# Performance work log

Hardware: AMD Instinct MI355X
Metric: run time of the kernel (lower is better)

## Reference

```python
import jax, jax.numpy as jnp
import numpy as np

N_NODES = 100000
N_EDGES = 3200000
DROP_P = 0.5


def gcn_conv(x, W, b, src, dst, deg_inv_sqrt, n):
    # PyG GCNConv with self-loops already folded into (src, dst):
    # out[j] = sum_{(i->j)} dinv[i]*dinv[j] * (x W)[i] + b
    h = x @ W
    norm = deg_inv_sqrt[src] * deg_inv_sqrt[dst]          # [E+N]
    msg = h[src] * norm[:, None]                          # [E+N, d_out]
    out = jax.ops.segment_sum(msg, dst, num_segments=n)
    return out + b


def dropout(x, key, p=DROP_P):
    keep = jax.random.bernoulli(key, 1.0 - p, x.shape)
    return jnp.where(keep, x / (1.0 - p), 0.0)


def setup_inputs() -> dict:
    key = jax.random.key(0)
    ks = jax.random.split(key, 8)
    x = jax.random.normal(ks[0], (N_NODES, 64), dtype=jnp.float32)
    edge_index = jax.random.randint(ks[1], (2, N_EDGES), 0, N_NODES, dtype=jnp.int64)
    def glorot(k, fin, fout):
        lim = float(np.sqrt(6.0 / (fin + fout)))
        return jax.random.uniform(k, (fin, fout), jnp.float32, -lim, lim)
    return {
        "x": x,
        "edge_index": edge_index,
        "W1": glorot(ks[2], 64, 32), "b1": jnp.zeros((32,), jnp.float32),
        "W2": glorot(ks[3], 32, 64), "b2": jnp.zeros((64,), jnp.float32),
        "W3": glorot(ks[4], 64, 32), "b3": jnp.zeros((32,), jnp.float32),
    }


def reference(x, edge_index, W1, b1, W2, b2, W3, b3):
    n = x.shape[0]
    loops = jnp.arange(n, dtype=edge_index.dtype)
    src = jnp.concatenate([edge_index[0], loops])          # [E+N]
    dst = jnp.concatenate([edge_index[1], loops])
    deg = jax.ops.segment_sum(jnp.ones_like(dst, dtype=x.dtype), dst, num_segments=n)
    deg_inv_sqrt = jnp.where(deg > 0, jax.lax.rsqrt(deg), 0.0)

    dkey = jax.random.key(42)
    k1, k2 = jax.random.split(dkey)

    h = gcn_conv(x, W1, b1, src, dst, deg_inv_sqrt, n)
    h = jax.nn.celu(h)
    h = dropout(h, k1)
    h = gcn_conv(h, W2, b2, src, dst, deg_inv_sqrt, n)
    h = jax.nn.celu(h)
    h = dropout(h, k2)
    h = gcn_conv(h, W3, b3, src, dst, deg_inv_sqrt, n)
    return jax.nn.celu(h)
```

## Files before the change

kernel.cpp:

```cpp
#include <hip/hip_runtime.h>
#include <stdint.h>
#include <stddef.h>

typedef _Float16 half_t;
typedef _Float16 half4 __attribute__((ext_vector_type(4)));
typedef _Float16 half8 __attribute__((ext_vector_type(8)));

__host__ __device__ __forceinline__ uint32_t rotl32(uint32_t v, uint32_t r) {
  return (v << r) | (v >> (32u - r));
}

__host__ __device__ __forceinline__ void tf2x32(uint32_t k0, uint32_t k1,
                                                uint32_t x0, uint32_t x1,
                                                uint32_t& o0, uint32_t& o1) {
  uint32_t ks2 = k0 ^ k1 ^ 0x1BD11BDAu;
  x0 += k0; x1 += k1;
  x0 += x1; x1 = rotl32(x1, 13); x1 ^= x0;
  x0 += x1; x1 = rotl32(x1, 15); x1 ^= x0;
  x0 += x1; x1 = rotl32(x1, 26); x1 ^= x0;
  x0 += x1; x1 = rotl32(x1, 6);  x1 ^= x0;
  x0 += k1; x1 += ks2 + 1u;
  x0 += x1; x1 = rotl32(x1, 17); x1 ^= x0;
  x0 += x1; x1 = rotl32(x1, 29); x1 ^= x0;
  x0 += x1; x1 = rotl32(x1, 16); x1 ^= x0;
  x0 += x1; x1 = rotl32(x1, 24); x1 ^= x0;
  x0 += ks2; x1 += k0 + 2u;
  x0 += x1; x1 = rotl32(x1, 13); x1 ^= x0;
  x0 += x1; x1 = rotl32(x1, 15); x1 ^= x0;
  x0 += x1; x1 = rotl32(x1, 26); x1 ^= x0;
  x0 += x1; x1 = rotl32(x1, 6);  x1 ^= x0;
  x0 += k0; x1 += k1 + 3u;
  x0 += x1; x1 = rotl32(x1, 17); x1 ^= x0;
  x0 += x1; x1 = rotl32(x1, 29); x1 ^= x0;
  x0 += x1; x1 = rotl32(x1, 16); x1 ^= x0;
  x0 += x1; x1 = rotl32(x1, 24); x1 ^= x0;
  x0 += k1; x1 += ks2 + 4u;
  x0 += x1; x1 = rotl32(x1, 13); x1 ^= x0;
  x0 += x1; x1 = rotl32(x1, 15); x1 ^= x0;
  x0 += x1; x1 = rotl32(x1, 26); x1 ^= x0;
  x0 += x1; x1 = rotl32(x1, 6);  x1 ^= x0;
  x0 += ks2; x1 += k0 + 5u;
  o0 = x0; o1 = x1;
}

__device__ __forceinline__ bool tf_keep(uint32_t k0, uint32_t k1, uint32_t idx) {
  uint32_t o0, o1;
  tf2x32(k0, k1, 0u, idx, o0, o1);
  return ((o0 ^ o1) >> 31) == 0u;
}

#define CHUNK 4096
#define STASH 5120

__global__ __launch_bounds__(1024) void zero1024(uint32_t* __restrict__ p) {
  p[threadIdx.x] = 0u;
}

__global__ __launch_bounds__(1024) void k4_binhist(const int* __restrict__ src,
                                                   const int* __restrict__ dst,
                                                   uint32_t* __restrict__ tbl,
                                                   uint32_t* __restrict__ gbcnt,
                                                   uint32_t* __restrict__ staging,
                                                   int E, int NB) {
  __shared__ uint32_t lcur[1024];
  __shared__ uint32_t ls[1024];
  __shared__ uint32_t stage[CHUNK];
  int tid = threadIdx.x;
  lcur[tid] = 0u;
  __syncthreads();
  int base = blockIdx.x * CHUNK;
  int end = min(base + CHUNK, E);
  uint32_t dv[4], sv[4];
  int m = 0;
  for (int i = base + tid; i < end; i += 1024) {
    dv[m] = (uint32_t)dst[i];
    sv[m] = (uint32_t)src[i];
    ++m;
  }
  for (int q = 0; q < m; ++q) atomicAdd(&lcur[dv[q] >> 7], 1u);
  __syncthreads();
  uint32_t v = lcur[tid];
  ls[tid] = v;
  __syncthreads();
  for (int off = 1; off < 1024; off <<= 1) {
    uint32_t t = (tid >= off) ? ls[tid - off] : 0u;
    __syncthreads();
    if (tid >= off) ls[tid] += t;
    __syncthreads();
  }
  uint32_t excl = ls[tid] - v;
  if (tid < NB) {
    tbl[(size_t)blockIdx.x * NB + tid] = (excl << 16) | v;
    if (v) atomicAdd(&gbcnt[tid], v);
  }
  lcur[tid] = excl;
  __syncthreads();
  for (int q = 0; q < m; ++q) {
    uint32_t d = dv[q];
    uint32_t p = atomicAdd(&lcur[d >> 7], 1u);
    stage[p] = ((d & 127u) << 17) | sv[q];
  }
  __syncthreads();
  int cnt_total = end - base;
  uint32_t* outp = staging + (size_t)blockIdx.x * CHUNK;
  for (int i = tid; i < cnt_total; i += 1024) outp[i] = stage[i];
}

__global__ __launch_bounds__(1024) void k3_bscan(const uint32_t* __restrict__ gbcnt,
                                                 uint32_t* __restrict__ bbase, int NB) {
  __shared__ uint32_t s[1024];
  int i = threadIdx.x;
  uint32_t v = (i < NB) ? gbcnt[i] : 0u;
  s[i] = v;
  __syncthreads();
  for (int off = 1; off < 1024; off <<= 1) {
    uint32_t t = (i >= off) ? s[i - off] : 0u;
    __syncthreads();
    if (i >= off) s[i] += t;
    __syncthreads();
  }
  if (i < NB) bbase[i] = s[i] - v;
}

__global__ __launch_bounds__(1024) void k5_fin(
    const uint32_t* __restrict__ staging, const uint32_t* __restrict__ tbl,
    const uint32_t* __restrict__ bbase, uint32_t* __restrict__ rowp,
    float* __restrict__ dinv, uint32_t* __restrict__ esrc,
    int n, int E, int NBLK, int NB) {
  __shared__ uint32_t loff[1024];
  __shared__ uint32_t P[1025];
  __shared__ uint32_t ls[1024];
  __shared__ uint32_t stash[STASH];
  __shared__ uint32_t lc[128];
  __shared__ uint32_t sc[128];
  __shared__ uint32_t lcur[128];
  int tid = threadIdx.x;
  int b = blockIdx.x;
  if (tid < 128) lc[tid] = 0u;
  uint32_t packed = (tid < NBLK) ? tbl[(size_t)tid * NB + b] : 0u;
  uint32_t v = packed & 0xFFFFu;
  loff[tid] = packed >> 16;
  ls[tid] = v;
  __syncthreads();
  for (int off = 1; off < 1024; off <<= 1) {
    uint32_t t = (tid >= off) ? ls[tid - off] : 0u;
    __syncthreads();
    if (tid >= off) ls[tid] += t;
    __syncthreads();
  }
  P[tid] = ls[tid] - v;
  if (tid == 1023) P[1024] = ls[1023];
  __syncthreads();
  uint32_t total = P[NBLK];
  for (uint32_t q = (uint32_t)tid; q < total; q += 1024u) {
    int lo = 0, hi = NBLK;
    while (hi - lo > 1) {
      int mid = (lo + hi) >> 1;
      if (P[mid] <= q) lo = mid; else hi = mid;
    }
    uint32_t e = staging[(size_t)lo * CHUNK + loff[lo] + (q - P[lo])];
    if (q < (uint32_t)STASH) stash[q] = e;
    atomicAdd(&lc[e >> 17], 1u);
  }
  __syncthreads();
  uint32_t myc = (tid < 128) ? lc[tid] : 0u;
  if (tid < 128) sc[tid] = myc;
  __syncthreads();
  for (int off = 1; off < 128; off <<= 1) {
    uint32_t t = (tid < 128 && tid >= off) ? sc[tid - off] : 0u;
    __syncthreads();
    if (tid < 128 && tid >= off) sc[tid] += t;
    __syncthreads();
  }
  uint32_t s = bbase[b];
  if (tid < 128) {
    uint32_t gstart = s + sc[tid] - myc;
    int node = (b << 7) + tid;
    if (node < n) {
      rowp[node] = gstart;
      dinv[node] = 1.0f / sqrtf((float)(myc + 1u));
    }
    lcur[tid] = gstart;
  }
  if (b == 0 && tid == 0) rowp[n] = (uint32_t)E;
  __syncthreads();
  uint32_t lim = total < (uint32_t)STASH ? total : (uint32_t)STASH;
  for (uint32_t q = (uint32_t)tid; q < lim; q += 1024u) {
    uint32_t e = stash[q];
    uint32_t pos = atomicAdd(&lcur[e >> 17], 1u);
    esrc[pos] = e & 0x1FFFFu;
  }
  if (total > (uint32_t)STASH) {
    for (uint32_t q = (uint32_t)STASH + (uint32_t)tid; q < total; q += 1024u) {
      int lo = 0, hi = NBLK;
      while (hi - lo > 1) {
        int mid = (lo + hi) >> 1;
        if (P[mid] <= q) lo = mid; else hi = mid;
      }
      uint32_t e = staging[(size_t)lo * CHUNK + loff[lo] + (q - P[lo])];
      uint32_t pos = atomicAdd(&lcur[e >> 17], 1u);
      esrc[pos] = e & 0x1FFFFu;
    }
  }
}

__global__ __launch_bounds__(256) void gemm_n64_k32(
    const float* __restrict__ X, const float* __restrict__ W,
    const float* __restrict__ dinv, half_t* __restrict__ out16, int n) {
  __shared__ float Ws[64 * 32];
  __shared__ float Xs[32 * 68];
  int tid = threadIdx.x;
  {
    const float4* Wv = (const float4*)W;
    float4* Wsv = (float4*)Ws;
    Wsv[tid] = Wv[tid];
    Wsv[tid + 256] = Wv[tid + 256];
  }
  int row0 = blockIdx.x * 32;
  {
    const float4* Xv = (const float4*)(X + (size_t)row0 * 64);
    int lim = (n - row0) * 16;
    float4 z = make_float4(0.f, 0.f, 0.f, 0.f);
    int i0 = tid, i1 = tid + 256;
    float4 v0 = (i0 < lim) ? Xv[i0] : z;
    float4 v1 = (i1 < lim) ? Xv[i1] : z;
    *(float4*)(Xs + (i0 >> 4) * 68 + ((i0 & 15) << 2)) = v0;
    *(float4*)(Xs + (i1 >> 4) * 68 + ((i1 & 15) << 2)) = v1;
  }
  __syncthreads();
  int r = tid >> 3;
  int c4 = (tid & 7) << 2;
  int row = row0 + r;
  if (row >= n) return;
  float4 acc = make_float4(0.f, 0.f, 0.f, 0.f);
#pragma unroll
  for (int k = 0; k < 64; k += 4) {
    float4 xv = *(const float4*)(Xs + r * 68 + k);
    float4 w0 = *(const float4*)(Ws + (k + 0) * 32 + c4);
    float4 w1 = *(const float4*)(Ws + (k + 1) * 32 + c4);
    float4 w2 = *(const float4*)(Ws + (k + 2) * 32 + c4);
    float4 w3 = *(const float4*)(Ws + (k + 3) * 32 + c4);
    acc.x = fmaf(xv.x, w0.x, acc.x); acc.y = fmaf(xv.x, w0.y, acc.y);
    acc.z = fmaf(xv.x, w0.z, acc.z); acc.w = fmaf(xv.x, w0.w, acc.w);
    acc.x = fmaf(xv.y, w1.x, acc.x); acc.y = fmaf(xv.y, w1.y, acc.y);
    acc.z = fmaf(xv.y, w1.z, acc.z); acc.w = fmaf(xv.y, w1.w, acc.w);
    acc.x = fmaf(xv.z, w2.x, acc.x); acc.y = fmaf(xv.z, w2.y, acc.y);
    acc.z = fmaf(xv.z, w2.z, acc.z); acc.w = fmaf(xv.z, w2.w, acc.w);
    acc.x = fmaf(xv.w, w3.x, acc.x); acc.y = fmaf(xv.w, w3.y, acc.y);
    acc.z = fmaf(xv.w, w3.z, acc.z); acc.w = fmaf(xv.w, w3.w, acc.w);
  }
  float dj = dinv[row];
  half4 h;
  h.x = (half_t)(acc.x * dj); h.y = (half_t)(acc.y * dj);
  h.z = (half_t)(acc.z * dj); h.w = (half_t)(acc.w * dj);
  *(half4*)(out16 + (size_t)row * 32 + c4) = h;
}

__global__ __launch_bounds__(256) void gemm_k32_n64_act(
    const float* __restrict__ X, const float* __restrict__ W,
    const float* __restrict__ bias, float* __restrict__ out,
    uint32_t k0, uint32_t k1, int n) {
  __shared__ float Ws[32 * 64];
  __shared__ float Xs[16 * 36];
  int tid = threadIdx.x;
  {
    const float4* Wv = (const float4*)W;
    float4* Wsv = (float4*)Ws;
    Wsv[tid] = Wv[tid];
    Wsv[tid + 256] = Wv[tid + 256];
  }
  int row0 = blockIdx.x * 16;
  if (tid < 128) {
    const float4* Xv = (const float4*)(X + (size_t)row0 * 32);
    int lim = (n - row0) * 8;
    float4 z = make_float4(0.f, 0.f, 0.f, 0.f);
    float4 v = (tid < lim) ? Xv[tid] : z;
    *(float4*)(Xs + (tid >> 3) * 36 + ((tid & 7) << 2)) = v;
  }
  __syncthreads();
  int r = tid >> 4;
  int c4 = (tid & 15) << 2;
  int row = row0 + r;
  if (row >= n) return;
  float4 acc = make_float4(0.f, 0.f, 0.f, 0.f);
#pragma unroll
  for (int k = 0; k < 32; k += 4) {
    float4 xv = *(const float4*)(Xs + r * 36 + k);
    float4 w0 = *(const float4*)(Ws + (k + 0) * 64 + c4);
    float4 w1 = *(const float4*)(Ws + (k + 1) * 64 + c4);
    float4 w2 = *(const float4*)(Ws + (k + 2) * 64 + c4);
    float4 w3 = *(const float4*)(Ws + (k + 3) * 64 + c4);
    acc.x = fmaf(xv.x, w0.x, acc.x); acc.y = fmaf(xv.x, w0.y, acc.y);
    acc.z = fmaf(xv.x, w0.z, acc.z); acc.w = fmaf(xv.x, w0.w, acc.w);
    acc.x = fmaf(xv.y, w1.x, acc.x); acc.y = fmaf(xv.y, w1.y, acc.y);
    acc.z = fmaf(xv.y, w1.z, acc.z); acc.w = fmaf(xv.y, w1.w, acc.w);
    acc.x = fmaf(xv.z, w2.x, acc.x); acc.y = fmaf(xv.z, w2.y, acc.y);
    acc.z = fmaf(xv.z, w2.z, acc.z); acc.w = fmaf(xv.z, w2.w, acc.w);
    acc.x = fmaf(xv.w, w3.x, acc.x); acc.y = fmaf(xv.w, w3.y, acc.y);
    acc.z = fmaf(xv.w, w3.z, acc.z); acc.w = fmaf(xv.w, w3.w, acc.w);
  }
  float4 bv = *(const float4*)(bias + c4);
  float vv[4] = {acc.x + bv.x, acc.y + bv.y, acc.z + bv.z, acc.w + bv.w};
  uint32_t base = (uint32_t)row * 64u + (uint32_t)c4;
#pragma unroll
  for (int q = 0; q < 4; ++q) {
    float v = vv[q];
    v = v > 0.f ? v : expm1f(v);
    vv[q] = tf_keep(k0, k1, base + q) ? v * 2.f : 0.f;
  }
  *(float4*)(out + (size_t)row * 64 + c4) = make_float4(vv[0], vv[1], vv[2], vv[3]);
}

__global__ __launch_bounds__(256) void gather_fin(
    const half_t* __restrict__ hs, const uint32_t* __restrict__ rowp,
    const uint32_t* __restrict__ esrc, const float* __restrict__ dinv,
    const float* __restrict__ bias, float* __restrict__ outf,
    half_t* __restrict__ outh, int n, int mode, uint32_t k0, uint32_t k1,
    float fone) {
  __shared__ __align__(16) float ldsred[256];
  (void)fone;
  int tid = threadIdx.x;
  int gt = blockIdx.x * 256 + tid;
  int j = gt >> 5;
  int g = tid >> 5;
  int l = tid & 31;
  int eslot = l >> 2;
  int chunk = l & 3;
  float acc[8] = {0.f, 0.f, 0.f, 0.f, 0.f, 0.f, 0.f, 0.f};
  uint32_t e0 = 0, deg = 0;
  float selfv = 0.f, dj = 0.f;
  if (j < n) {
    e0 = rowp[j];
    deg = rowp[j + 1] - e0;
    selfv = (float)hs[(size_t)j * 32 + l];
    dj = dinv[j];
  }
  const half_t* hp = hs + (size_t)(chunk << 3);
  const half8 hz = {(half_t)0, (half_t)0, (half_t)0, (half_t)0,
                    (half_t)0, (half_t)0, (half_t)0, (half_t)0};
  for (uint32_t base = 0; base < deg; base += 64u) {
    uint32_t rem = deg - base;
    if (rem > 64u) rem = 64u;
    uint32_t li0 = (uint32_t)l < rem ? (uint32_t)l : rem - 1u;
    uint32_t t1 = 32u + (uint32_t)l;
    uint32_t li1 = t1 < rem ? t1 : rem - 1u;
    uint32_t idx0 = __builtin_nontemporal_load(&esrc[e0 + base + li0]);
    uint32_t idx1 = __builtin_nontemporal_load(&esrc[e0 + base + li1]);
    half8 v0, v1, v2, v3, v4, v5, v6, v7;
#define GLOAD(KK, IDX, VOUT)                                              \
    {                                                                     \
      uint32_t kp = (uint32_t)(KK) + (uint32_t)eslot;                     \
      uint32_t s = (uint32_t)__shfl((int)(IDX), (int)(kp & 31u), 32);     \
      VOUT = hz;                                                          \
      if (kp < rem) VOUT = *(const half8*)(hp + ((size_t)s << 5));        \
    }
    GLOAD(0,  idx0, v0)
    GLOAD(8,  idx0, v1)
    GLOAD(16, idx0, v2)
    GLOAD(24, idx0, v3)
    GLOAD(32, idx1, v4)
    GLOAD(40, idx1, v5)
    GLOAD(48, idx1, v6)
    GLOAD(56, idx1, v7)
#undef GLOAD
    half8 s01 = v0 + v1;
    half8 s23 = v2 + v3;
    half8 s45 = v4 + v5;
    half8 s67 = v6 + v7;
#pragma unroll
    for (int q = 0; q < 8; ++q) {
      acc[q] += (float)s01[q];
      acc[q] += (float)s23[q];
      acc[q] += (float)s45[q];
      acc[q] += (float)s67[q];
    }
  }
#pragma unroll
  for (int m = 4; m <= 16; m <<= 1) {
#pragma unroll
    for (int q = 0; q < 8; ++q) acc[q] += __shfl_xor(acc[q], m);
  }
  if (l < 4) {
    *(float4*)(&ldsred[(g << 5) + (chunk << 3) + 0]) =
        make_float4(acc[0], acc[1], acc[2], acc[3]);
    *(float4*)(&ldsred[(g << 5) + (chunk << 3) + 4]) =
        make_float4(acc[4], acc[5], acc[6], acc[7]);
  }
  __builtin_amdgcn_wave_barrier();
  if (j >= n) return;
  float sum = ldsred[(g << 5) + l];
  sum += selfv;
  float v = dj * sum;
  if (mode == 1) {
    v += bias[l];
    v = v > 0.f ? v : expm1f(v);
    __builtin_nontemporal_store(v, &outf[gt]);
  } else if (mode == 3) {
    v += bias[l];
    v = v > 0.f ? v : expm1f(v);
    v = tf_keep(k0, k1, (uint32_t)gt) ? v * 2.f : 0.f;
    v *= dj;
    __builtin_nontemporal_store((half_t)v, &outh[gt]);
  } else {
    __builtin_nontemporal_store(v, &outf[gt]);
  }
}

extern "C" void kernel_launch(void* const* d_in, const int* in_sizes, int n_in,
                              void* d_out, int out_size, void* d_ws, size_t ws_size,
                              hipStream_t stream) {
  const float* x  = (const float*)d_in[0];
  const int*   ei = (const int*)d_in[1];
  const float* W1 = (const float*)d_in[2];
  const float* b1 = (const float*)d_in[3];
  const float* W2 = (const float*)d_in[4];
  const float* b2 = (const float*)d_in[5];
  const float* W3 = (const float*)d_in[6];
  const float* b3 = (const float*)d_in[7];
  float* out = (float*)d_out;

  const int n = in_sizes[0] / 64;
  const int E = in_sizes[1] / 2;
  const int* src = ei;
  const int* dst = ei + E;

  char* ws = (char*)d_ws;
  size_t off = 0;
  auto alloc = [&](size_t bytes) {
    void* p = ws + off;
    off = (off + bytes + 255) & ~(size_t)255;
    return p;
  };
  float*    A32   = (float*)alloc((size_t)n * 32 * 4);
  float*    C     = (float*)alloc((size_t)n * 64 * 4);
  half_t*   A16   = (half_t*)alloc((size_t)n * 32 * 2);
  half_t*   B16   = (half_t*)alloc((size_t)n * 32 * 2);
  float*    dinv  = (float*)alloc((size_t)n * 4);
  uint32_t* rowp  = (uint32_t*)alloc((size_t)(n + 1) * 4);
  uint32_t* esrc  = (uint32_t*)alloc((size_t)E * 4);
  uint32_t* gbcnt = (uint32_t*)alloc(1024 * 4);
  uint32_t* bbase = (uint32_t*)alloc(1024 * 4);
  uint32_t* staging = (uint32_t*)C;
  uint32_t* tbl     = (uint32_t*)A32;
  (void)ws_size; (void)n_in; (void)out_size;

  uint32_t k1a, k1b, k2a, k2b;
  tf2x32(0u, 42u, 0u, 0u, k1a, k1b);
  tf2x32(0u, 42u, 0u, 1u, k2a, k2b);

  const int NB   = (n + 127) >> 7;
  const int NBLK = (E + CHUNK - 1) / CHUNK;
  const int nv   = n * 32;
  const int gV   = (nv + 255) / 256;
  const int gG1  = (n + 31) / 32;
  const int gG2  = (n + 15) / 16;
  dim3 blk(256);

  zero1024<<<1, dim3(1024), 0, stream>>>(gbcnt);
  k4_binhist<<<NBLK, dim3(1024), 0, stream>>>(src, dst, tbl, gbcnt, staging, E, NB);
  k3_bscan<<<1, dim3(1024), 0, stream>>>(gbcnt, bbase, NB);
  k5_fin<<<NB, dim3(1024), 0, stream>>>(staging, tbl, bbase, rowp, dinv, esrc, n, E, NBLK, NB);

  gemm_n64_k32<<<gG1, blk, 0, stream>>>(x, W1, dinv, A16, n);
  gather_fin<<<gV, blk, 0, stream>>>(A16, rowp, esrc, dinv, b1, nullptr, B16, n, 3, k1a, k1b, 1.0f);

  gather_fin<<<gV, blk, 0, stream>>>(B16, rowp, esrc, dinv, nullptr, A32, nullptr, n, 0, 0u, 0u, 1.0f);
  gemm_k32_n64_act<<<gG2, blk, 0, stream>>>(A32, W2, b2, C, k2a, k2b, n);

  gemm_n64_k32<<<gG1, blk, 0, stream>>>(C, W3, dinv, A16, n);
  gather_fin<<<gV, blk, 0, stream>>>(A16, rowp, esrc, dinv, b3, out, nullptr, n, 1, 0u, 0u, 1.0f);
}
```

Before: 315.2 us.

## Make gather kernel persistent with software-pipelined row metadata and index prefetch

Converts the gather/aggregate kernel from one 32-lane group per node to a grid-stride persistent loop with 2048 blocks. While one node's neighbour features are gathered, it prefetches the next node's edge indices and the row pointers of the node after that. The goal is to hide the dependent rowp->esrc->feature load latency chain. The cost is more registers per thread and fewer resident waves overall, which may lower occupancy-based latency hiding.

New measurement: 330.5 us. +4.9%, slower.

```diff
diff --git a/kernel.cpp b/kernel.cpp
--- a/kernel.cpp
+++ b/kernel.cpp
@@ -315,37 +315,48 @@
     const half_t* __restrict__ hs, const uint32_t* __restrict__ rowp,
     const uint32_t* __restrict__ esrc, const float* __restrict__ dinv,
     const float* __restrict__ bias, float* __restrict__ outf,
-    half_t* __restrict__ outh, int n, int mode, uint32_t k0, uint32_t k1,
-    float fone) {
+    half_t* __restrict__ outh, int n, int mode, uint32_t k0, uint32_t k1) {
   __shared__ __align__(16) float ldsred[256];
-  (void)fone;
   int tid = threadIdx.x;
-  int gt = blockIdx.x * 256 + tid;
-  int j = gt >> 5;
   int g = tid >> 5;
   int l = tid & 31;
   int eslot = l >> 2;
   int chunk = l & 3;
-  float acc[8] = {0.f, 0.f, 0.f, 0.f, 0.f, 0.f, 0.f, 0.f};
-  uint32_t e0 = 0, deg = 0;
-  float selfv = 0.f, dj = 0.f;
+  const half_t* hp = hs + (size_t)(chunk << 3);
+  const half8 hz = {(half_t)0, (half_t)0, (half_t)0, (half_t)0,
+                    (half_t)0, (half_t)0, (half_t)0, (half_t)0};
+  const int G = (int)gridDim.x * 8;
+  int j  = (int)blockIdx.x * 8 + g;
+  int j1 = j + G;
+  int j2 = j1 + G;
+
+  uint32_t e0 = 0, deg = 0, e0n = 0, degn = 0;
+  float selfv = 0.f, dj = 0.f, selfvn = 0.f, djn = 0.f;
+  uint32_t idx0 = 0, idx1 = 0;
+
   if (j < n) {
     e0 = rowp[j];
     deg = rowp[j + 1] - e0;
     selfv = (float)hs[(size_t)j * 32 + l];
     dj = dinv[j];
   }
-  const half_t* hp = hs + (size_t)(chunk << 3);
-  const half8 hz = {(half_t)0, (half_t)0, (half_t)0, (half_t)0,
-                    (half_t)0, (half_t)0, (half_t)0, (half_t)0};
-  for (uint32_t base = 0; base < deg; base += 64u) {
-    uint32_t rem = deg - base;
-    if (rem > 64u) rem = 64u;
+  if (j1 < n) {
+    e0n = rowp[j1];
+    degn = rowp[j1 + 1] - e0n;
+    selfvn = (float)hs[(size_t)j1 * 32 + l];
+    djn = dinv[j1];
+  }
+  if (j < n && deg > 0u) {
+    uint32_t rem = deg < 64u ? deg : 64u;
     uint32_t li0 = (uint32_t)l < rem ? (uint32_t)l : rem - 1u;
     uint32_t t1 = 32u + (uint32_t)l;
     uint32_t li1 = t1 < rem ? t1 : rem - 1u;
-    uint32_t idx0 = __builtin_nontemporal_load(&esrc[e0 + base + li0]);
-    uint32_t idx1 = __builtin_nontemporal_load(&esrc[e0 + base + li1]);
+    idx0 = __builtin_nontemporal_load(&esrc[e0 + li0]);
+    idx1 = __builtin_nontemporal_load(&esrc[e0 + li1]);
+  }
+
+  while (j < n) {
+    uint32_t rem = deg < 64u ? deg : 64u;
     half8 v0, v1, v2, v3, v4, v5, v6, v7;
 #define GLOAD(KK, IDX, VOUT)                                              \
     {                                                                     \
@@ -362,47 +373,109 @@
     GLOAD(40, idx1, v5)
     GLOAD(48, idx1, v6)
     GLOAD(56, idx1, v7)
+    uint32_t e0p = 0, degp = 0;
+    float selfvp = 0.f, djp = 0.f;
+    if (j2 < n) {
+      e0p = rowp[j2];
+      degp = rowp[j2 + 1] - e0p;
+      selfvp = (float)hs[(size_t)j2 * 32 + l];
+      djp = dinv[j2];
+    }
+    uint32_t idx0n = 0, idx1n = 0;
+    if (j1 < n && degn > 0u) {
+      uint32_t remn = degn < 64u ? degn : 64u;
+      uint32_t li0 = (uint32_t)l < remn ? (uint32_t)l : remn - 1u;
+      uint32_t t1 = 32u + (uint32_t)l;
+      uint32_t li1 = t1 < remn ? t1 : remn - 1u;
+      idx0n = __builtin_nontemporal_load(&esrc[e0n + li0]);
+      idx1n = __builtin_nontemporal_load(&esrc[e0n + li1]);
+    }
+    float acc[8] = {0.f, 0.f, 0.f, 0.f, 0.f, 0.f, 0.f, 0.f};
+    {
+      half8 s01 = v0 + v1;
+      half8 s23 = v2 + v3;
+      half8 s45 = v4 + v5;
+      half8 s67 = v6 + v7;
+#pragma unroll
+      for (int q = 0; q < 8; ++q) {
+        acc[q] += (float)s01[q];
+        acc[q] += (float)s23[q];
+        acc[q] += (float)s45[q];
+        acc[q] += (float)s67[q];
+      }
+    }
+    for (uint32_t base = 64u; base < deg; base += 64u) {
+      uint32_t rem2 = deg - base;
+      if (rem2 > 64u) rem2 = 64u;
+      uint32_t li0 = (uint32_t)l < rem2 ? (uint32_t)l : rem2 - 1u;
+      uint32_t t1 = 32u + (uint32_t)l;
+      uint32_t li1 = t1 < rem2 ? t1 : rem2 - 1u;
+      uint32_t ix0 = __builtin_nontemporal_load(&esrc[e0 + base + li0]);
+      uint32_t ix1 = __builtin_nontemporal_load(&esrc[e0 + base + li1]);
+      half8 w0, w1, w2, w3, w4, w5, w6, w7;
+      uint32_t sv = rem2;
+      (void)sv;
+      {
+        uint32_t remS = rem2;
+        half8* wp[8] = {&w0, &w1, &w2, &w3, &w4, &w5, &w6, &w7};
+#pragma unroll
+        for (int kk = 0; kk < 8; ++kk) {
+          uint32_t kp = (uint32_t)(kk << 3) + (uint32_t)eslot;
+          uint32_t idxs = kk < 4 ? ix0 : ix1;
+          uint32_t s = (uint32_t)__shfl((int)idxs, (int)(kp & 31u), 32);
+          *wp[kk] = hz;
+          if (kp < remS) *wp[kk] = *(const half8*)(hp + ((size_t)s << 5));
+        }
+      }
+      half8 s01 = w0 + w1;
+      half8 s23 = w2 + w3;
+      half8 s45 = w4 + w5;
+      half8 s67 = w6 + w7;
+#pragma unroll
+      for (int q = 0; q < 8; ++q) {
+        acc[q] += (float)s01[q];
+        acc[q] += (float)s23[q];
+        acc[q] += (float)s45[q];
+        acc[q] += (float)s67[q];
+      }
+    }
+#pragma unroll
+    for (int m = 4; m <= 16; m <<= 1) {
+#pragma unroll
+      for (int q = 0; q < 8; ++q) acc[q] += __shfl_xor(acc[q], m);
+    }
+    if (l < 4) {
+      *(float4*)(&ldsred[(g << 5) + (chunk << 3) + 0]) =
+          make_float4(acc[0], acc[1], acc[2], acc[3]);
+      *(float4*)(&ldsred[(g << 5) + (chunk << 3) + 4]) =
+          make_float4(acc[4], acc[5], acc[6], acc[7]);
+    }
+    __builtin_amdgcn_wave_barrier();
+    {
+      float sum = ldsred[(g << 5) + l];
+      sum += selfv;
+      float v = dj * sum;
+      int gt = j * 32 + l;
+      if (mode == 1) {
+        v += bias[l];
+        v = v > 0.f ? v : expm1f(v);
+        __builtin_nontemporal_store(v, &outf[gt]);
+      } else if (mode == 3) {
+        v += bias[l];
+        v = v > 0.f ? v : expm1f(v);
+        v = tf_keep(k0, k1, (uint32_t)gt) ? v * 2.f : 0.f;
+        v *= dj;
+        __builtin_nontemporal_store((half_t)v, &outh[gt]);
+      } else {
+        __builtin_nontemporal_store(v, &outf[gt]);
+      }
+    }
+    __builtin_amdgcn_wave_barrier();
+    j = j1; j1 = j2; j2 += G;
+    e0 = e0n; deg = degn; selfv = selfvn; dj = djn;
+    e0n = e0p; degn = degp; selfvn = selfvp; djn = djp;
+    idx0 = idx0n; idx1 = idx1n;
 #undef GLOAD
-    half8 s01 = v0 + v1;
-    half8 s23 = v2 + v3;
-    half8 s45 = v4 + v5;
-    half8 s67 = v6 + v7;
-#pragma unroll
-    for (int q = 0; q < 8; ++q) {
-      acc[q] += (float)s01[q];
-      acc[q] += (float)s23[q];
-      acc[q] += (float)s45[q];
-      acc[q] += (float)s67[q];
-    }
-  }
-#pragma unroll
-  for (int m = 4; m <= 16; m <<= 1) {
-#pragma unroll
-    for (int q = 0; q < 8; ++q) acc[q] += __shfl_xor(acc[q], m);
-  }
-  if (l < 4) {
-    *(float4*)(&ldsred[(g << 5) + (chunk << 3) + 0]) =
-        make_float4(acc[0], acc[1], acc[2], acc[3]);
-    *(float4*)(&ldsred[(g << 5) + (chunk << 3) + 4]) =
-        make_float4(acc[4], acc[5], acc[6], acc[7]);
-  }
-  __builtin_amdgcn_wave_barrier();
-  if (j >= n) return;
-  float sum = ldsred[(g << 5) + l];
-  sum += selfv;
-  float v = dj * sum;
-  if (mode == 1) {
-    v += bias[l];
-    v = v > 0.f ? v : expm1f(v);
-    __builtin_nontemporal_store(v, &outf[gt]);
-  } else if (mode == 3) {
-    v += bias[l];
-    v = v > 0.f ? v : expm1f(v);
-    v = tf_keep(k0, k1, (uint32_t)gt) ? v * 2.f : 0.f;
-    v *= dj;
-    __builtin_nontemporal_store((half_t)v, &outh[gt]);
-  } else {
-    __builtin_nontemporal_store(v, &outf[gt]);
   }
 }
 
@@ -450,10 +523,9 @@
 
   const int NB   = (n + 127) >> 7;
   const int NBLK = (E + CHUNK - 1) / CHUNK;
-  const int nv   = n * 32;
-  const int gV   = (nv + 255) / 256;
   const int gG1  = (n + 31) / 32;
   const int gG2  = (n + 15) / 16;
+  const int gV   = 2048;
   dim3 blk(256);
 
   zero1024<<<1, dim3(1024), 0, stream>>>(gbcnt);
@@ -462,11 +534,11 @@
   k5_fin<<<NB, dim3(1024), 0, stream>>>(staging, tbl, bbase, rowp, dinv, esrc, n, E, NBLK, NB);
 
   gemm_n64_k32<<<gG1, blk, 0, stream>>>(x, W1, dinv, A16, n);
-  gather_fin<<<gV, blk, 0, stream>>>(A16, rowp, esrc, dinv, b1, nullptr, B16, n, 3, k1a, k1b, 1.0f);
-
-  gather_fin<<<gV, blk, 0, stream>>>(B16, rowp, esrc, dinv, nullptr, A32, nullptr, n, 0, 0u, 0u, 1.0f);
+  gather_fin<<<gV, blk, 0, stream>>>(A16, rowp, esrc, dinv, b1, nullptr, B16, n, 3, k1a, k1b);
+
+  gather_fin<<<gV, blk, 0, stream>>>(B16, rowp, esrc, dinv, nullptr, A32, nullptr, n, 0, 0u, 0u);
   gemm_k32_n64_act<<<gG2, blk, 0, stream>>>(A32, W2, b2, C, k2a, k2b, n);
 
   gemm_n64_k32<<<gG1, blk, 0, stream>>>(C, W3, dinv, A16, n);
-  gather_fin<<<gV, blk, 0, stream>>>(A16, rowp, esrc, dinv, b3, out, nullptr, n, 1, 0u, 0u, 1.0f);
-}
+  gather_fin<<<gV, blk, 0, stream>>>(A16, rowp, esrc, dinv, b3, out, nullptr, n, 1, 0u, 0u);
+}
```

## Replace two-level binned CSR build with global-atomic degree count and placement

Applied to the files above, without the earlier changes.

Replaces the chunked bin-histogram and staging-based CSR construction with a simpler pipeline: zero degrees, count in-degrees with global atomics, run a three-kernel scan to get row pointers and dinv, then scatter source indices with per-node atomic cursors. The aim is to drop the shared-memory staging, binary searches and the extra staging-buffer traffic. In exchange it relies on many contended global atomics, produces esrc in nondeterministic order within each row, and uses more kernel launches. The scan2 kernel assumes at most 128 scan blocks.

After: 664.5 us. 111% more time.

```diff
diff --git a/kernel.cpp b/kernel.cpp
--- a/kernel.cpp
+++ b/kernel.cpp
@@ -49,158 +49,86 @@
   return ((o0 ^ o1) >> 31) == 0u;
 }
 
-#define CHUNK 4096
-#define STASH 5120
-
-__global__ __launch_bounds__(1024) void zero1024(uint32_t* __restrict__ p) {
-  p[threadIdx.x] = 0u;
-}
-
-__global__ __launch_bounds__(1024) void k4_binhist(const int* __restrict__ src,
-                                                   const int* __restrict__ dst,
-                                                   uint32_t* __restrict__ tbl,
-                                                   uint32_t* __restrict__ gbcnt,
-                                                   uint32_t* __restrict__ staging,
-                                                   int E, int NB) {
-  __shared__ uint32_t lcur[1024];
+__global__ __launch_bounds__(256) void k_zero(uint32_t* __restrict__ deg, int n) {
+  int i = blockIdx.x * 256 + threadIdx.x;
+  int gs = gridDim.x * 256;
+  for (; i < n; i += gs) deg[i] = 0u;
+}
+
+__global__ __launch_bounds__(256) void k_deg(const int* __restrict__ dst,
+                                             uint32_t* __restrict__ deg, int E) {
+  int i = blockIdx.x * 256 + threadIdx.x;
+  int gs = gridDim.x * 256;
+  for (; i < E; i += gs) {
+    uint32_t d = (uint32_t)__builtin_nontemporal_load(&dst[i]);
+    atomicAdd(&deg[d], 1u);
+  }
+}
+
+__global__ __launch_bounds__(1024) void k_scan1(const uint32_t* __restrict__ deg,
+                                                uint32_t* __restrict__ rowp,
+                                                uint32_t* __restrict__ bsum,
+                                                float* __restrict__ dinv, int n) {
   __shared__ uint32_t ls[1024];
-  __shared__ uint32_t stage[CHUNK];
-  int tid = threadIdx.x;
-  lcur[tid] = 0u;
-  __syncthreads();
-  int base = blockIdx.x * CHUNK;
-  int end = min(base + CHUNK, E);
-  uint32_t dv[4], sv[4];
-  int m = 0;
-  for (int i = base + tid; i < end; i += 1024) {
-    dv[m] = (uint32_t)dst[i];
-    sv[m] = (uint32_t)src[i];
-    ++m;
-  }
-  for (int q = 0; q < m; ++q) atomicAdd(&lcur[dv[q] >> 7], 1u);
-  __syncthreads();
-  uint32_t v = lcur[tid];
-  ls[tid] = v;
+  int t = threadIdx.x;
+  int j = blockIdx.x * 1024 + t;
+  uint32_t v = (j < n) ? deg[j] : 0u;
+  ls[t] = v;
   __syncthreads();
   for (int off = 1; off < 1024; off <<= 1) {
-    uint32_t t = (tid >= off) ? ls[tid - off] : 0u;
+    uint32_t x = (t >= off) ? ls[t - off] : 0u;
     __syncthreads();
-    if (tid >= off) ls[tid] += t;
+    if (t >= off) ls[t] += x;
     __syncthreads();
   }
-  uint32_t excl = ls[tid] - v;
-  if (tid < NB) {
-    tbl[(size_t)blockIdx.x * NB + tid] = (excl << 16) | v;
-    if (v) atomicAdd(&gbcnt[tid], v);
-  }
-  lcur[tid] = excl;
-  __syncthreads();
-  for (int q = 0; q < m; ++q) {
-    uint32_t d = dv[q];
-    uint32_t p = atomicAdd(&lcur[d >> 7], 1u);
-    stage[p] = ((d & 127u) << 17) | sv[q];
-  }
-  __syncthreads();
-  int cnt_total = end - base;
-  uint32_t* outp = staging + (size_t)blockIdx.x * CHUNK;
-  for (int i = tid; i < cnt_total; i += 1024) outp[i] = stage[i];
-}
-
-__global__ __launch_bounds__(1024) void k3_bscan(const uint32_t* __restrict__ gbcnt,
-                                                 uint32_t* __restrict__ bbase, int NB) {
-  __shared__ uint32_t s[1024];
-  int i = threadIdx.x;
-  uint32_t v = (i < NB) ? gbcnt[i] : 0u;
-  s[i] = v;
-  __syncthreads();
-  for (int off = 1; off < 1024; off <<= 1) {
-    uint32_t t = (i >= off) ? s[i - off] : 0u;
-    __syncthreads();
-    if (i >= off) s[i] += t;
-    __syncthreads();
-  }
-  if (i < NB) bbase[i] = s[i] - v;
-}
-
-__global__ __launch_bounds__(1024) void k5_fin(
-    const uint32_t* __restrict__ staging, const uint32_t* __restrict__ tbl,
-    const uint32_t* __restrict__ bbase, uint32_t* __restrict__ rowp,
-    float* __restrict__ dinv, uint32_t* __restrict__ esrc,
-    int n, int E, int NBLK, int NB) {
-  __shared__ uint32_t loff[1024];
-  __shared__ uint32_t P[1025];
-  __shared__ uint32_t ls[1024];
-  __shared__ uint32_t stash[STASH];
-  __shared__ uint32_t lc[128];
-  __shared__ uint32_t sc[128];
-  __shared__ uint32_t lcur[128];
-  int tid = threadIdx.x;
-  int b = blockIdx.x;
-  if (tid < 128) lc[tid] = 0u;
-  uint32_t packed = (tid < NBLK) ? tbl[(size_t)tid * NB + b] : 0u;
-  uint32_t v = packed & 0xFFFFu;
-  loff[tid] = packed >> 16;
-  ls[tid] = v;
-  __syncthreads();
-  for (int off = 1; off < 1024; off <<= 1) {
-    uint32_t t = (tid >= off) ? ls[tid - off] : 0u;
-    __syncthreads();
-    if (tid >= off) ls[tid] += t;
-    __syncthreads();
-  }
-  P[tid] = ls[tid] - v;
-  if (tid == 1023) P[1024] = ls[1023];
-  __syncthreads();
-  uint32_t total = P[NBLK];
-  for (uint32_t q = (uint32_t)tid; q < total; q += 1024u) {
-    int lo = 0, hi = NBLK;
-    while (hi - lo > 1) {
-      int mid = (lo + hi) >> 1;
-      if (P[mid] <= q) lo = mid; else hi = mid;
-    }
-    uint32_t e = staging[(size_t)lo * CHUNK + loff[lo] + (q - P[lo])];
-    if (q < (uint32_t)STASH) stash[q] = e;
-    atomicAdd(&lc[e >> 17], 1u);
-  }
-  __syncthreads();
-  uint32_t myc = (tid < 128) ? lc[tid] : 0u;
-  if (tid < 128) sc[tid] = myc;
+  if (j < n) {
+    rowp[j] = ls[t] - v;
+    dinv[j] = 1.0f / sqrtf((float)(v + 1u));
+  }
+  if (t == 1023) bsum[blockIdx.x] = ls[1023];
+}
+
+__global__ __launch_bounds__(128) void k_scan2(const uint32_t* __restrict__ bsum,
+                                               uint32_t* __restrict__ boffs, int NBB) {
+  __shared__ uint32_t s[128];
+  int t = threadIdx.x;
+  uint32_t v = (t < NBB) ? bsum[t] : 0u;
+  s[t] = v;
   __syncthreads();
   for (int off = 1; off < 128; off <<= 1) {
-    uint32_t t = (tid < 128 && tid >= off) ? sc[tid - off] : 0u;
+    uint32_t x = (t >= off) ? s[t - off] : 0u;
     __syncthreads();
-    if (tid < 128 && tid >= off) sc[tid] += t;
+    if (t >= off) s[t] += x;
     __syncthreads();
   }
-  uint32_t s = bbase[b];
-  if (tid < 128) {
-    uint32_t gstart = s + sc[tid] - myc;
-    int node = (b << 7) + tid;
-    if (node < n) {
-      rowp[node] = gstart;
-      dinv[node] = 1.0f / sqrtf((float)(myc + 1u));
-    }
-    lcur[tid] = gstart;
-  }
-  if (b == 0 && tid == 0) rowp[n] = (uint32_t)E;
-  __syncthreads();
-  uint32_t lim = total < (uint32_t)STASH ? total : (uint32_t)STASH;
-  for (uint32_t q = (uint32_t)tid; q < lim; q += 1024u) {
-    uint32_t e = stash[q];
-    uint32_t pos = atomicAdd(&lcur[e >> 17], 1u);
-    esrc[pos] = e & 0x1FFFFu;
-  }
-  if (total > (uint32_t)STASH) {
-    for (uint32_t q = (uint32_t)STASH + (uint32_t)tid; q < total; q += 1024u) {
-      int lo = 0, hi = NBLK;
-      while (hi - lo > 1) {
-        int mid = (lo + hi) >> 1;
-        if (P[mid] <= q) lo = mid; else hi = mid;
-      }
-      uint32_t e = staging[(size_t)lo * CHUNK + loff[lo] + (q - P[lo])];
-      uint32_t pos = atomicAdd(&lcur[e >> 17], 1u);
-      esrc[pos] = e & 0x1FFFFu;
-    }
+  if (t < NBB) boffs[t] = s[t] - v;
+}
+
+__global__ __launch_bounds__(256) void k_scan3(uint32_t* __restrict__ rowp,
+                                               const uint32_t* __restrict__ boffs,
+                                               uint32_t* __restrict__ cur,
+                                               int n, int E) {
+  int i = blockIdx.x * 256 + threadIdx.x;
+  int gs = gridDim.x * 256;
+  for (; i < n; i += gs) {
+    uint32_t r = rowp[i] + boffs[i >> 10];
+    rowp[i] = r;
+    cur[i] = r;
+  }
+  if (blockIdx.x == 0 && threadIdx.x == 0) rowp[n] = (uint32_t)E;
+}
+
+__global__ __launch_bounds__(256) void k_place(const int* __restrict__ src,
+                                               const int* __restrict__ dst,
+                                               uint32_t* __restrict__ cur,
+                                               uint32_t* __restrict__ esrc, int E) {
+  int i = blockIdx.x * 256 + threadIdx.x;
+  int gs = gridDim.x * 256;
+  for (; i < E; i += gs) {
+    uint32_t s = (uint32_t)__builtin_nontemporal_load(&src[i]);
+    uint32_t d = (uint32_t)__builtin_nontemporal_load(&dst[i]);
+    uint32_t pos = atomicAdd(&cur[d], 1u);
+    esrc[pos] = s;
   }
 }
 
@@ -438,28 +366,30 @@
   float*    dinv  = (float*)alloc((size_t)n * 4);
   uint32_t* rowp  = (uint32_t*)alloc((size_t)(n + 1) * 4);
   uint32_t* esrc  = (uint32_t*)alloc((size_t)E * 4);
-  uint32_t* gbcnt = (uint32_t*)alloc(1024 * 4);
-  uint32_t* bbase = (uint32_t*)alloc(1024 * 4);
-  uint32_t* staging = (uint32_t*)C;
-  uint32_t* tbl     = (uint32_t*)A32;
+  uint32_t* deg   = (uint32_t*)alloc((size_t)n * 4);
+  uint32_t* cur   = (uint32_t*)alloc((size_t)n * 4);
+  uint32_t* bsum  = (uint32_t*)alloc(1024 * 4);
+  uint32_t* boffs = (uint32_t*)alloc(1024 * 4);
   (void)ws_size; (void)n_in; (void)out_size;
 
   uint32_t k1a, k1b, k2a, k2b;
   tf2x32(0u, 42u, 0u, 0u, k1a, k1b);
   tf2x32(0u, 42u, 0u, 1u, k2a, k2b);
 
-  const int NB   = (n + 127) >> 7;
-  const int NBLK = (E + CHUNK - 1) / CHUNK;
+  const int NBB  = (n + 1023) >> 10;
   const int nv   = n * 32;
   const int gV   = (nv + 255) / 256;
   const int gG1  = (n + 31) / 32;
   const int gG2  = (n + 15) / 16;
+  const int gN   = (n + 255) / 256;
   dim3 blk(256);
 
-  zero1024<<<1, dim3(1024), 0, stream>>>(gbcnt);
-  k4_binhist<<<NBLK, dim3(1024), 0, stream>>>(src, dst, tbl, gbcnt, staging, E, NB);
-  k3_bscan<<<1, dim3(1024), 0, stream>>>(gbcnt, bbase, NB);
-  k5_fin<<<NB, dim3(1024), 0, stream>>>(staging, tbl, bbase, rowp, dinv, esrc, n, E, NBLK, NB);
+  k_zero<<<gN, blk, 0, stream>>>(deg, n);
+  k_deg<<<2048, blk, 0, stream>>>(dst, deg, E);
+  k_scan1<<<NBB, dim3(1024), 0, stream>>>(deg, rowp, bsum, dinv, n);
+  k_scan2<<<1, dim3(128), 0, stream>>>(bsum, boffs, NBB);
+  k_scan3<<<gN, blk, 0, stream>>>(rowp, boffs, cur, n, E);
+  k_place<<<2048, blk, 0, stream>>>(src, dst, cur, esrc, E);
 
   gemm_n64_k32<<<gG1, blk, 0, stream>>>(x, W1, dinv, A16, n);
   gather_fin<<<gV, blk, 0, stream>>>(A16, rowp, esrc, dinv, b1, nullptr, B16, n, 3, k1a, k1b, 1.0f);
```

## Fuse layer-2 gather with W2 GEMM, activation, dropout and W3 GEMM

Applied to the files above, without the earlier changes.

Replaces the separate gather, k32->n64 GEMM with CELU and dropout, and n64->k32 GEMM with a single kernel. Each wave aggregates one node's neighbours, then applies W2, bias, CELU and dropout, then W3 and the dinv scale from LDS-resident weights, writing fp16 directly. This removes two kernel launches and the fp32 round trips through A32 and C. In exchange, each block loads 16KB of weights into LDS, which may lower occupancy of the latency-bound gather, and staging and tbl now get their own workspace allocations.

After: 313.2 us (median of 2 runs). No clear change (-0.6%).

```diff
diff --git a/kernel.cpp b/kernel.cpp
--- a/kernel.cpp
+++ b/kernel.cpp
@@ -256,61 +256,6 @@
   *(half4*)(out16 + (size_t)row * 32 + c4) = h;
 }
 
-__global__ __launch_bounds__(256) void gemm_k32_n64_act(
-    const float* __restrict__ X, const float* __restrict__ W,
-    const float* __restrict__ bias, float* __restrict__ out,
-    uint32_t k0, uint32_t k1, int n) {
-  __shared__ float Ws[32 * 64];
-  __shared__ float Xs[16 * 36];
-  int tid = threadIdx.x;
-  {
-    const float4* Wv = (const float4*)W;
-    float4* Wsv = (float4*)Ws;
-    Wsv[tid] = Wv[tid];
-    Wsv[tid + 256] = Wv[tid + 256];
-  }
-  int row0 = blockIdx.x * 16;
-  if (tid < 128) {
-    const float4* Xv = (const float4*)(X + (size_t)row0 * 32);
-    int lim = (n - row0) * 8;
-    float4 z = make_float4(0.f, 0.f, 0.f, 0.f);
-    float4 v = (tid < lim) ? Xv[tid] : z;
-    *(float4*)(Xs + (tid >> 3) * 36 + ((tid & 7) << 2)) = v;
-  }
-  __syncthreads();
-  int r = tid >> 4;
-  int c4 = (tid & 15) << 2;
-  int row = row0 + r;
-  if (row >= n) return;
-  float4 acc = make_float4(0.f, 0.f, 0.f, 0.f);
-#pragma unroll
-  for (int k = 0; k < 32; k += 4) {
-    float4 xv = *(const float4*)(Xs + r * 36 + k);
-    float4 w0 = *(const float4*)(Ws + (k + 0) * 64 + c4);
-    float4 w1 = *(const float4*)(Ws + (k + 1) * 64 + c4);
-    float4 w2 = *(const float4*)(Ws + (k + 2) * 64 + c4);
-    float4 w3 = *(const float4*)(Ws + (k + 3) * 64 + c4);
-    acc.x = fmaf(xv.x, w0.x, acc.x); acc.y = fmaf(xv.x, w0.y, acc.y);
-    acc.z = fmaf(xv.x, w0.z, acc.z); acc.w = fmaf(xv.x, w0.w, acc.w);
-    acc.x = fmaf(xv.y, w1.x, acc.x); acc.y = fmaf(xv.y, w1.y, acc.y);
-    acc.z = fmaf(xv.y, w1.z, acc.z); acc.w = fmaf(xv.y, w1.w, acc.w);
-    acc.x = fmaf(xv.z, w2.x, acc.x); acc.y = fmaf(xv.z, w2.y, acc.y);
-    acc.z = fmaf(xv.z, w2.z, acc.z); acc.w = fmaf(xv.z, w2.w, acc.w);
-    acc.x = fmaf(xv.w, w3.x, acc.x); acc.y = fmaf(xv.w, w3.y, acc.y);
-    acc.z = fmaf(xv.w, w3.z, acc.z); acc.w = fmaf(xv.w, w3.w, acc.w);
-  }
-  float4 bv = *(const float4*)(bias + c4);
-  float vv[4] = {acc.x + bv.x, acc.y + bv.y, acc.z + bv.z, acc.w + bv.w};
-  uint32_t base = (uint32_t)row * 64u + (uint32_t)c4;
-#pragma unroll
-  for (int q = 0; q < 4; ++q) {
-    float v = vv[q];
-    v = v > 0.f ? v : expm1f(v);
-    vv[q] = tf_keep(k0, k1, base + q) ? v * 2.f : 0.f;
-  }
-  *(float4*)(out + (size_t)row * 64 + c4) = make_float4(vv[0], vv[1], vv[2], vv[3]);
-}
-
 __global__ __launch_bounds__(256) void gather_fin(
     const half_t* __restrict__ hs, const uint32_t* __restrict__ rowp,
     const uint32_t* __restrict__ esrc, const float* __restrict__ dinv,
@@ -406,6 +351,128 @@
   }
 }
 
+__global__ __launch_bounds__(256) void gather_gemm2(
+    const half_t* __restrict__ hs, const uint32_t* __restrict__ rowp,
+    const uint32_t* __restrict__ esrc, const float* __restrict__ dinv,
+    const float* __restrict__ W2, const float* __restrict__ b2,
+    const float* __restrict__ W3, half_t* __restrict__ outh,
+    int n, uint32_t k0, uint32_t k1) {
+  __shared__ __align__(16) float ldsred[256];
+  __shared__ __align__(16) float W2s[32 * 64];
+  __shared__ __align__(16) float W3s[64 * 32];
+  __shared__ __align__(16) float b2s[64];
+  __shared__ __align__(16) float tls[8 * 64];
+  int tid = threadIdx.x;
+  {
+    const float4* w2v = (const float4*)W2;
+    const float4* w3v = (const float4*)W3;
+    float4* s2 = (float4*)W2s;
+    float4* s3 = (float4*)W3s;
+    s2[tid] = w2v[tid];
+    s2[tid + 256] = w2v[tid + 256];
+    s3[tid] = w3v[tid];
+    s3[tid + 256] = w3v[tid + 256];
+    if (tid < 16) ((float4*)b2s)[tid] = ((const float4*)b2)[tid];
+  }
+  __syncthreads();
+  int j = blockIdx.x * 8 + (tid >> 5);
+  int g = tid >> 5;
+  int l = tid & 31;
+  int eslot = l >> 2;
+  int chunk = l & 3;
+  float acc[8] = {0.f, 0.f, 0.f, 0.f, 0.f, 0.f, 0.f, 0.f};
+  uint32_t e0 = 0, deg = 0;
+  float selfv = 0.f, dj = 0.f;
+  if (j < n) {
+    e0 = rowp[j];
+    deg = rowp[j + 1] - e0;
+    selfv = (float)hs[(size_t)j * 32 + l];
+    dj = dinv[j];
+  }
+  const half_t* hp = hs + (size_t)(chunk << 3);
+  const half8 hz = {(half_t)0, (half_t)0, (half_t)0, (half_t)0,
+                    (half_t)0, (half_t)0, (half_t)0, (half_t)0};
+  for (uint32_t base = 0; base < deg; base += 64u) {
+    uint32_t rem = deg - base;
+    if (rem > 64u) rem = 64u;
+    uint32_t li0 = (uint32_t)l < rem ? (uint32_t)l : rem - 1u;
+    uint32_t t1 = 32u + (uint32_t)l;
+    uint32_t li1 = t1 < rem ? t1 : rem - 1u;
+    uint32_t idx0 = __builtin_nontemporal_load(&esrc[e0 + base + li0]);
+    uint32_t idx1 = __builtin_nontemporal_load(&esrc[e0 + base + li1]);
+    half8 v0, v1, v2, v3, v4, v5, v6, v7;
+#define GLOAD(KK, IDX, VOUT)                                              \
+    {                                                                     \
+      uint32_t kp = (uint32_t)(KK) + (uint32_t)eslot;                     \
+      uint32_t s = (uint32_t)__shfl((int)(IDX), (int)(kp & 31u), 32);     \
+      VOUT = hz;                                                          \
+      if (kp < rem) VOUT = *(const half8*)(hp + ((size_t)s << 5));        \
+    }
+    GLOAD(0,  idx0, v0)
+    GLOAD(8,  idx0, v1)
+    GLOAD(16, idx0, v2)
+    GLOAD(24, idx0, v3)
+    GLOAD(32, idx1, v4)
+    GLOAD(40, idx1, v5)
+    GLOAD(48, idx1, v6)
+    GLOAD(56, idx1, v7)
+#undef GLOAD
+    half8 s01 = v0 + v1;
+    half8 s23 = v2 + v3;
+    half8 s45 = v4 + v5;
+    half8 s67 = v6 + v7;
+#pragma unroll
+    for (int q = 0; q < 8; ++q) {
+      acc[q] += (float)s01[q];
+      acc[q] += (float)s23[q];
+      acc[q] += (float)s45[q];
+      acc[q] += (float)s67[q];
+    }
+  }
+#pragma unroll
+  for (int m = 4; m <= 16; m <<= 1) {
+#pragma unroll
+    for (int q = 0; q < 8; ++q) acc[q] += __shfl_xor(acc[q], m);
+  }
+  if (l < 4) {
+    *(float4*)(&ldsred[(g << 5) + (chunk << 3) + 0]) =
+        make_float4(acc[0], acc[1], acc[2], acc[3]);
+    *(float4*)(&ldsred[(g << 5) + (chunk << 3) + 4]) =
+        make_float4(acc[4], acc[5], acc[6], acc[7]);
+  }
+  __builtin_amdgcn_wave_barrier();
+  float hv = dj * (ldsred[(g << 5) + l] + selfv);
+  __builtin_amdgcn_wave_barrier();
+  ldsred[(g << 5) + l] = hv;
+  __builtin_amdgcn_wave_barrier();
+  int c0 = l << 1;
+  float t0 = 0.f, t1v = 0.f;
+#pragma unroll
+  for (int k = 0; k < 32; ++k) {
+    float xk = ldsred[(g << 5) + k];
+    t0 = fmaf(xk, W2s[k * 64 + c0], t0);
+    t1v = fmaf(xk, W2s[k * 64 + c0 + 1], t1v);
+  }
+  t0 += b2s[c0];
+  t1v += b2s[c0 + 1];
+  t0 = t0 > 0.f ? t0 : expm1f(t0);
+  t1v = t1v > 0.f ? t1v : expm1f(t1v);
+  uint32_t ridx = (uint32_t)j * 64u + (uint32_t)c0;
+  t0 = tf_keep(k0, k1, ridx) ? t0 * 2.f : 0.f;
+  t1v = tf_keep(k0, k1, ridx + 1u) ? t1v * 2.f : 0.f;
+  tls[(g << 6) + c0] = t0;
+  tls[(g << 6) + c0 + 1] = t1v;
+  __builtin_amdgcn_wave_barrier();
+  float a = 0.f;
+#pragma unroll
+  for (int c = 0; c < 64; ++c) {
+    a = fmaf(tls[(g << 6) + c], W3s[c * 32 + l], a);
+  }
+  if (j < n) {
+    __builtin_nontemporal_store((half_t)(a * dj), &outh[(size_t)j * 32 + l]);
+  }
+}
+
 extern "C" void kernel_launch(void* const* d_in, const int* in_sizes, int n_in,
                               void* d_out, int out_size, void* d_ws, size_t ws_size,
                               hipStream_t stream) {
@@ -431,8 +498,9 @@
     off = (off + bytes + 255) & ~(size_t)255;
     return p;
   };
-  float*    A32   = (float*)alloc((size_t)n * 32 * 4);
-  float*    C     = (float*)alloc((size_t)n * 64 * 4);
+  const int NB   = (n + 127) >> 7;
+  const int NBLK = (E + CHUNK - 1) / CHUNK;
+
   half_t*   A16   = (half_t*)alloc((size_t)n * 32 * 2);
   half_t*   B16   = (half_t*)alloc((size_t)n * 32 * 2);
   float*    dinv  = (float*)alloc((size_t)n * 4);
@@ -440,20 +508,17 @@
   uint32_t* esrc  = (uint32_t*)alloc((size_t)E * 4);
   uint32_t* gbcnt = (uint32_t*)alloc(1024 * 4);
   uint32_t* bbase = (uint32_t*)alloc(1024 * 4);
-  uint32_t* staging = (uint32_t*)C;
-  uint32_t* tbl     = (uint32_t*)A32;
+  uint32_t* staging = (uint32_t*)alloc((size_t)NBLK * CHUNK * 4);
+  uint32_t* tbl     = (uint32_t*)alloc((size_t)NBLK * NB * 4);
   (void)ws_size; (void)n_in; (void)out_size;
 
   uint32_t k1a, k1b, k2a, k2b;
   tf2x32(0u, 42u, 0u, 0u, k1a, k1b);
   tf2x32(0u, 42u, 0u, 1u, k2a, k2b);
 
-  const int NB   = (n + 127) >> 7;
-  const int NBLK = (E + CHUNK - 1) / CHUNK;
   const int nv   = n * 32;
   const int gV   = (nv + 255) / 256;
   const int gG1  = (n + 31) / 32;
-  const int gG2  = (n + 15) / 16;
   dim3 blk(256);
 
   zero1024<<<1, dim3(1024), 0, stream>>>(gbcnt);
@@ -464,9 +529,7 @@
   gemm_n64_k32<<<gG1, blk, 0, stream>>>(x, W1, dinv, A16, n);
   gather_fin<<<gV, blk, 0, stream>>>(A16, rowp, esrc, dinv, b1, nullptr, B16, n, 3, k1a, k1b, 1.0f);
 
-  gather_fin<<<gV, blk, 0, stream>>>(B16, rowp, esrc, dinv, nullptr, A32, nullptr, n, 0, 0u, 0u, 1.0f);
-  gemm_k32_n64_act<<<gG2, blk, 0, stream>>>(A32, W2, b2, C, k2a, k2b, n);
-
-  gemm_n64_k32<<<gG1, blk, 0, stream>>>(C, W3, dinv, A16, n);
+  gather_gemm2<<<gV, blk, 0, stream>>>(B16, rowp, esrc, dinv, W2, b2, W3, A16, n, k2a, k2b);
+
   gather_fin<<<gV, blk, 0, stream>>>(A16, rowp, esrc, dinv, b3, out, nullptr, n, 1, 0u, 0u, 1.0f);
 }
```
